# Performance work log

Measured on AMD Instinct MI355X. Metric: run time of the kernel, lower is better.

The kernel has to match this reference:

```python
import jax, jax.numpy as jnp
import numpy as np

EPS = 1e-5
GROUPS = 32
NH = 4


def group_norm(x, gamma, beta, groups=GROUPS, eps=EPS):
    # x: (B, C, H, W); normalize over (C//groups, H, W) per group
    B, C, H, W = x.shape
    xg = x.reshape(B, groups, C // groups, H, W)
    mean = xg.mean(axis=(2, 3, 4), keepdims=True)
    var = xg.var(axis=(2, 3, 4), keepdims=True)
    xn = ((xg - mean) * jax.lax.rsqrt(var + eps)).reshape(B, C, H, W)
    return xn * gamma[None, :, None, None] + beta[None, :, None, None]


def conv1x1(x, w, b):
    # x: (B, Cin, H, W), w: (Cout, Cin), b: (Cout,)
    return jnp.einsum('bchw,oc->bohw', x, w) + b[None, :, None, None]


def setup_inputs() -> dict:
    key = jax.random.key(0)
    ks = jax.random.split(key, 16)
    B, C, H, W = 4, 256, 64, 64
    d = {}
    d['x'] = jax.random.normal(ks[0], (B, C, H, W), jnp.float32)
    d['cond'] = jax.random.normal(ks[1], (B, C, H, W), jnp.float32)
    s = 1.0 / np.sqrt(C)
    d['gn_q_w'] = jnp.ones((C,), jnp.float32)
    d['gn_q_b'] = jnp.zeros((C,), jnp.float32)
    d['gn_kv_w'] = jnp.ones((C,), jnp.float32)
    d['gn_kv_b'] = jnp.zeros((C,), jnp.float32)
    d['wq'] = jax.random.normal(ks[2], (C, C), jnp.float32) * s
    d['bq'] = jnp.zeros((C,), jnp.float32)
    d['wk'] = jax.random.normal(ks[3], (C, C), jnp.float32) * s
    d['bk'] = jnp.zeros((C,), jnp.float32)
    d['wv'] = jax.random.normal(ks[4], (C, C), jnp.float32) * s
    d['bv'] = jnp.zeros((C,), jnp.float32)
    d['wo'] = jax.random.normal(ks[5], (C, C), jnp.float32) * s
    d['bo'] = jnp.zeros((C,), jnp.float32)
    return d


def reference(x, cond, gn_q_w, gn_q_b, gn_kv_w, gn_kv_b,
              wq, bq, wk, bk, wv, bv, wo, bo):
    B, C, H, W = x.shape
    hd = C // NH
    N = H * W
    scale = hd ** -0.5
    kv_in = group_norm(cond, gn_kv_w, gn_kv_b)
    q = conv1x1(group_norm(x, gn_q_w, gn_q_b), wq, bq)
    k = conv1x1(kv_in, wk, bk)
    v = conv1x1(kv_in, wv, bv)
    # (B, nh, head_dim, N) layout as in the original
    q = q.reshape(B, NH, hd, N)
    k = k.reshape(B, NH, hd, N)
    v = v.reshape(B, NH, hd, N)
    attn = jnp.einsum('bhdn,bhdm->bhnm', q, k) * scale
    attn = jax.nn.softmax(attn, axis=-1)
    out = jnp.einsum('bhnm,bhdm->bhdn', attn, v).reshape(B, C, H, W)
    return x + conv1x1(out, wo, bo)
```

## Files before the change

### kernel.cpp

```cpp
#include <hip/hip_runtime.h>
#include <hip/hip_bf16.h>

#define B_   4
#define C_   256
#define N_   4096
#define NH_  4
#define HD_  64
#define G_   32
#define CPG_ 8
#define EPS_ 1e-5f

typedef __bf16 bf16x8 __attribute__((ext_vector_type(8)));
typedef __bf16 bf16x4 __attribute__((ext_vector_type(4)));
typedef float  f32x4  __attribute__((ext_vector_type(4)));
typedef unsigned int u32x4 __attribute__((ext_vector_type(4)));
typedef unsigned int u32x2 __attribute__((ext_vector_type(2)));

#define EXP2F(x) __builtin_amdgcn_exp2f(x)

static __device__ __forceinline__ unsigned int packbf(float a, float b) {
    __bf16 x = (__bf16)a, y = (__bf16)b;
    unsigned short ux = __builtin_bit_cast(unsigned short, x);
    unsigned short uy = __builtin_bit_cast(unsigned short, y);
    return (unsigned int)ux | ((unsigned int)uy << 16);
}

__global__ __launch_bounds__(256) void wconv_kernel(const float* __restrict__ w0,
                                                    const float* __restrict__ w1,
                                                    const float* __restrict__ w2,
                                                    const float* __restrict__ w3,
                                                    __bf16* __restrict__ dst) {
    const float* srcs[4] = {w0, w1, w2, w3};
    const float* s = srcs[blockIdx.y];
    __bf16* d = dst + (size_t)blockIdx.y * C_ * C_;
    const int i = blockIdx.x * 256 + threadIdx.x;
    float4 v = ((const float4*)s)[i];
    bf16x4 o;
    o[0] = (__bf16)v.x; o[1] = (__bf16)v.y; o[2] = (__bf16)v.z; o[3] = (__bf16)v.w;
    ((bf16x4*)d)[i] = o;
}

__global__ __launch_bounds__(1024) void gn_stats_kernel(const float* __restrict__ in0,
                                                        const float* __restrict__ in1,
                                                        const float* __restrict__ gw0,
                                                        const float* __restrict__ gb0,
                                                        const float* __restrict__ gw1,
                                                        const float* __restrict__ gb1,
                                                        float* __restrict__ stat) {
    const int which = blockIdx.y;
    const float* in = which ? in1 : in0;
    const float* gw = which ? gw1 : gw0;
    const float* gb = which ? gb1 : gb0;
    const int b = blockIdx.x / G_;
    const int g = blockIdx.x % G_;
    const int tid = threadIdx.x;
    const size_t base = ((size_t)b * C_ + g * CPG_) * N_;
    const float4* pv = (const float4*)(in + base);
    const int NC = (CPG_ * N_) / 4;

    float s = 0.f, ss = 0.f;
    #pragma unroll
    for (int i = tid; i < NC; i += 1024) {
        float4 v = pv[i];
        s  += v.x + v.y + v.z + v.w;
        ss += v.x * v.x + v.y * v.y + v.z * v.z + v.w * v.w;
    }
    #pragma unroll
    for (int m = 32; m >= 1; m >>= 1) { s += __shfl_xor(s, m); ss += __shfl_xor(ss, m); }
    __shared__ float red[32];
    const int w = tid >> 6;
    if ((tid & 63) == 0) { red[w] = s; red[16 + w] = ss; }
    __syncthreads();
    s = 0.f; ss = 0.f;
    #pragma unroll
    for (int i = 0; i < 16; i++) { s += red[i]; ss += red[16 + i]; }
    const float mean = s * (1.f / 32768.f);
    const float var  = ss * (1.f / 32768.f) - mean * mean;
    const float rinv = rsqrtf(var + EPS_);
    if (tid < CPG_) {
        const int c = g * CPG_ + tid;
        float* sp = stat + (size_t)which * 2 * B_ * C_;
        const float sc = rinv * gw[c];
        sp[b * C_ + c] = sc;
        sp[B_ * C_ + b * C_ + c] = gb[c] - mean * sc;
    }
}

__global__ __launch_bounds__(256, 4) void gn_norm_kernel(const float* __restrict__ in0,
                                                         const float* __restrict__ in1,
                                                         const float* __restrict__ stat,
                                                         __bf16* __restrict__ out0,
                                                         __bf16* __restrict__ out1) {
    const int which = blockIdx.z;
    const float* in = which ? in1 : in0;
    __bf16* out = which ? out1 : out0;
    const int n0 = blockIdx.x * 64;
    const int b  = blockIdx.y;
    const int tid = threadIdx.x;
    const int w = tid >> 6, lane = tid & 63;
    const float* scp = stat + (size_t)which * 2 * B_ * C_ + b * C_;
    const float* shp = scp + B_ * C_;

    __shared__ __bf16 Lt[64][264];

    #pragma unroll 16
    for (int p = 0; p < 64; p++) {
        const int c = p * 4 + w;
        const float v = in[((size_t)(b * C_ + c)) * N_ + n0 + lane];
        const float o = v * scp[c] + shp[c];
        const int ch = (((c >> 3) ^ (lane >> 3)) << 3) + (c & 7);
        Lt[lane][ch] = (__bf16)o;
    }
    __syncthreads();
    #pragma unroll
    for (int q = 0; q < 8; q++) {
        const int r = q * 8 + (tid >> 5);
        const int l = tid & 31;
        const int ch = (l ^ (r >> 3)) << 3;
        *(bf16x8*)(out + ((size_t)b * N_ + n0 + r) * C_ + l * 8) =
            *(const bf16x8*)(&Lt[r][ch]);
    }
}

__global__ __launch_bounds__(256, 2) void qkv_kernel(const __bf16* __restrict__ Wall,
                                                     const float* __restrict__ bq,
                                                     const float* __restrict__ bk,
                                                     const float* __restrict__ bv,
                                                     const __bf16* __restrict__ Xq,
                                                     const __bf16* __restrict__ Xkv,
                                                     __bf16* __restrict__ Qo,
                                                     __bf16* __restrict__ Ko,
                                                     __bf16* __restrict__ Vo,
                                                     float qscale) {
    const int n0 = blockIdx.x * 64;
    const int sel = blockIdx.y >> 1;
    const int m0 = (blockIdx.y & 1) * 128;
    const int b  = blockIdx.z;
    const int tid = threadIdx.x;
    const int w = tid >> 6, lane = tid & 63, quad = lane >> 4, l16 = lane & 15;
    const int wn = (w >> 1) * 32;
    const int wm = (w & 1) * 64;

    const __bf16* Wb   = Wall + (size_t)sel * C_ * C_;
    const __bf16* XT   = (sel == 0) ? Xq : Xkv;
    const float*  bias = (sel == 0) ? bq : ((sel == 1) ? bk : bv);
    const float   psc  = (sel == 0) ? qscale : 1.0f;

    __shared__ union {
        __bf16 Wl[128][264];
        __bf16 T1[64][136];
        __bf16 Tv[128][72];
    } sm;

    const __bf16* wsrc = Wb + (size_t)m0 * C_;
    #pragma unroll
    for (int i = 0; i < 16; i++) {
        const int e = i * 256 + tid;
        const int row = e >> 5;
        const int c8 = (e & 31) * 8;
        *(bf16x8*)(&sm.Wl[row][c8]) = *(const bf16x8*)(wsrc + (size_t)row * C_ + c8);
    }

    const __bf16* ap0 = XT + ((size_t)b * N_ + n0 + wn + l16) * C_ + quad * 8;
    const __bf16* ap1 = ap0 + (size_t)16 * C_;
    bf16x8 areg[2][8];
    #pragma unroll
    for (int ks = 0; ks < 8; ks++) {
        areg[0][ks] = *(const bf16x8*)(ap0 + ks * 32);
        areg[1][ks] = *(const bf16x8*)(ap1 + ks * 32);
    }

    f32x4 acc[2][4];
    #pragma unroll
    for (int qg = 0; qg < 2; qg++)
        #pragma unroll
        for (int jm = 0; jm < 4; jm++) acc[qg][jm] = (f32x4){0.f, 0.f, 0.f, 0.f};

    __syncthreads();

    #pragma unroll
    for (int ks = 0; ks < 8; ks++) {
        const int kc = ks * 32;
        #pragma unroll
        for (int jm = 0; jm < 4; jm++) {
            bf16x8 bw = *(const bf16x8*)(&sm.Wl[wm + jm * 16 + l16][kc + quad * 8]);
            acc[0][jm] = __builtin_amdgcn_mfma_f32_16x16x32_bf16(areg[0][ks], bw, acc[0][jm], 0, 0, 0);
            acc[1][jm] = __builtin_amdgcn_mfma_f32_16x16x32_bf16(areg[1][ks], bw, acc[1][jm], 0, 0, 0);
        }
    }

    if (sel == 2) {
        __syncthreads();
        #pragma unroll
        for (int qg = 0; qg < 2; qg++)
            #pragma unroll
            for (int jm = 0; jm < 4; jm++) {
                const int mm = wm + jm * 16 + l16;
                const int nn = wn + qg * 16 + quad * 4;
                const float bi = bias[m0 + mm];
                bf16x4 o;
                #pragma unroll
                for (int r = 0; r < 4; r++) o[r] = (__bf16)(acc[qg][jm][r] + bi);
                *(bf16x4*)(&sm.Tv[mm][nn]) = o;
            }
        __syncthreads();
        #pragma unroll
        for (int i = 0; i < 4; i++) {
            const int mrow = i * 32 + (tid >> 3);
            const int ch = (tid & 7) * 8;
            *(bf16x8*)(Vo + (size_t)(b * C_ + m0 + mrow) * N_ + n0 + ch) =
                *(const bf16x8*)(&sm.Tv[mrow][ch]);
        }
    } else {
        __bf16* OUTb = (sel == 0) ? Qo : Ko;
        __syncthreads();
        #pragma unroll
        for (int qg = 0; qg < 2; qg++)
            #pragma unroll
            for (int jm = 0; jm < 4; jm++) {
                const int m = m0 + wm + jm * 16 + l16;
                const float bi = bias[m];
                #pragma unroll
                for (int r = 0; r < 4; r++)
                    sm.T1[wn + qg * 16 + quad * 4 + r][wm + jm * 16 + l16] =
                        (__bf16)((acc[qg][jm][r] + bi) * psc);
            }
        __syncthreads();
        const int h0 = m0 >> 6;
        #pragma unroll
        for (int i = 0; i < 4; i++) {
            const int idx = i * 256 + tid;
            const int row = idx >> 4;
            const int c = (idx & 15) * 8;
            const int hh = h0 + (c >> 6);
            const int d = c & 63;
            *(bf16x8*)(OUTb + ((size_t)(b * NH_ + hh) * N_ + n0 + row) * HD_ + d) =
                *(const bf16x8*)(&sm.T1[row][c]);
        }
    }
}

__global__ __launch_bounds__(256, 2) void gemm_kernel(const __bf16* __restrict__ Wb,
                                                      const float* __restrict__ bias,
                                                      const __bf16* __restrict__ XT,
                                                      float* __restrict__ OUTf,
                                                      const float* __restrict__ RES) {
    const int n0 = blockIdx.x * 64;
    const int m0 = blockIdx.y * 128;
    const int b  = blockIdx.z;
    const int tid = threadIdx.x;
    const int w = tid >> 6, lane = tid & 63, quad = lane >> 4, l16 = lane & 15;
    const int wn = (w >> 1) * 32;
    const int wm = (w & 1) * 64;

    __shared__ union {
        __bf16 Wl[128][264];
        float  Tf[128][68];
    } sm;

    const __bf16* wsrc = Wb + (size_t)m0 * C_;
    #pragma unroll
    for (int i = 0; i < 16; i++) {
        const int e = i * 256 + tid;
        const int row = e >> 5;
        const int c8 = (e & 31) * 8;
        *(bf16x8*)(&sm.Wl[row][c8]) = *(const bf16x8*)(wsrc + (size_t)row * C_ + c8);
    }

    const __bf16* ap0 = XT + ((size_t)b * N_ + n0 + wn + l16) * C_ + quad * 8;
    const __bf16* ap1 = ap0 + (size_t)16 * C_;
    bf16x8 areg[2][8];
    #pragma unroll
    for (int ks = 0; ks < 8; ks++) {
        areg[0][ks] = *(const bf16x8*)(ap0 + ks * 32);
        areg[1][ks] = *(const bf16x8*)(ap1 + ks * 32);
    }

    f32x4 acc[2][4];
    #pragma unroll
    for (int qg = 0; qg < 2; qg++)
        #pragma unroll
        for (int jm = 0; jm < 4; jm++) acc[qg][jm] = (f32x4){0.f, 0.f, 0.f, 0.f};

    __syncthreads();

    #pragma unroll
    for (int ks = 0; ks < 8; ks++) {
        const int kc = ks * 32;
        #pragma unroll
        for (int jm = 0; jm < 4; jm++) {
            bf16x8 bw = *(const bf16x8*)(&sm.Wl[wm + jm * 16 + l16][kc + quad * 8]);
            acc[0][jm] = __builtin_amdgcn_mfma_f32_16x16x32_bf16(areg[0][ks], bw, acc[0][jm], 0, 0, 0);
            acc[1][jm] = __builtin_amdgcn_mfma_f32_16x16x32_bf16(areg[1][ks], bw, acc[1][jm], 0, 0, 0);
        }
    }

    __syncthreads();
    #pragma unroll
    for (int qg = 0; qg < 2; qg++)
        #pragma unroll
        for (int jm = 0; jm < 4; jm++) {
            const int mm = wm + jm * 16 + l16;
            const int nn = wn + qg * 16 + quad * 4;
            const float bi = bias[m0 + mm];
            f32x4 o;
            #pragma unroll
            for (int r = 0; r < 4; r++) o[r] = acc[qg][jm][r] + bi;
            *(f32x4*)(&sm.Tf[mm][nn]) = o;
        }
    __syncthreads();
    #pragma unroll
    for (int qp = 0; qp < 8; qp++) {
        const int mrow = qp * 16 + (tid >> 4);
        const int k4 = (tid & 15) * 4;
        const size_t off = (size_t)(b * C_ + m0 + mrow) * N_ + n0 + k4;
        const float4 res = *(const float4*)(RES + off);
        f32x4 v = *(const f32x4*)(&sm.Tf[mrow][k4]);
        v[0] += res.x; v[1] += res.y; v[2] += res.z; v[3] += res.w;
        *(f32x4*)(OUTf + off) = v;
    }
}

__global__ __launch_bounds__(256, 2) void attn_kernel(const __bf16* __restrict__ qT,
                                                      const __bf16* __restrict__ kT,
                                                      const __bf16* __restrict__ V,
                                                      __bf16* __restrict__ O) {
    const int flat = blockIdx.y * 32 + blockIdx.x;
    const int bh = flat & 15;
    const int qt = flat >> 4;
    const int q0 = qt * 128;
    const int b = bh >> 2, h = bh & 3;
    const int tid = threadIdx.x;
    const int w = tid >> 6, lane = tid & 63, quad = lane >> 4, l16 = lane & 15;

    __shared__ union SMem {
        struct { __bf16 K[2][64][72]; __bf16 Vt[2][64][72]; } kv;
        __bf16 Ot[128][72];
    } sm;

    const __bf16* qTb = qT + (size_t)bh * N_ * HD_;
    const __bf16* kTb = kT + (size_t)bh * N_ * HD_;
    const __bf16* Vb  = V + ((size_t)b * C_ + h * HD_) * N_;

    bf16x8 qa[2][2];
    #pragma unroll
    for (int qg = 0; qg < 2; qg++)
        #pragma unroll
        for (int kk = 0; kk < 2; kk++)
            qa[qg][kk] = *(const bf16x8*)(qTb + (size_t)(q0 + w * 32 + qg * 16 + l16) * HD_ + kk * 32 + quad * 8);

    f32x4 oacc[2][4];
    #pragma unroll
    for (int qg = 0; qg < 2; qg++)
        #pragma unroll
        for (int j = 0; j < 4; j++) oacc[qg][j] = (f32x4){0.f, 0.f, 0.f, 0.f};
    float lsum[2] = {0.f, 0.f};

    const int srow = tid >> 3;
    const int scol = (tid & 7) * 8;

    bf16x8 rk[2], rv[2];
    #pragma unroll
    for (int i = 0; i < 2; i++) {
        const int row = srow + i * 32;
        rk[i] = *(const bf16x8*)(kTb + (size_t)row * HD_ + scol);
        rv[i] = *(const bf16x8*)(Vb + (size_t)row * N_ + scol);
    }

    for (int it = 0; it < N_ / 64; it++) {
        const int cur = it & 1;
        const int nm0 = ((it + 1) * 64) & (N_ - 1);
        #pragma unroll
        for (int i = 0; i < 2; i++) {
            const int row = srow + i * 32;
            *(bf16x8*)(&sm.kv.K[cur][row][scol])  = rk[i];
            *(bf16x8*)(&sm.kv.Vt[cur][row][scol]) = rv[i];
        }
        #pragma unroll
        for (int i = 0; i < 2; i++) {
            const int row = srow + i * 32;
            rk[i] = *(const bf16x8*)(kTb + (size_t)(nm0 + row) * HD_ + scol);
            rv[i] = *(const bf16x8*)(Vb + (size_t)row * N_ + nm0 + scol);
        }
        asm volatile("s_waitcnt lgkmcnt(0)" ::: "memory");
        __builtin_amdgcn_s_barrier();
        bf16x8 kb[2][4], vb[2][4];
        #pragma unroll
        for (int kk = 0; kk < 2; kk++)
            #pragma unroll
            for (int j = 0; j < 4; j++) {
                kb[kk][j] = *(const bf16x8*)(&sm.kv.K[cur][j * 16 + l16][kk * 32 + quad * 8]);
                vb[kk][j] = *(const bf16x8*)(&sm.kv.Vt[cur][j * 16 + l16][kk * 32 + quad * 8]);
            }
        #pragma unroll
        for (int qg = 0; qg < 2; qg++) {
            f32x4 s[4];
            #pragma unroll
            for (int j = 0; j < 4; j++) s[j] = (f32x4){0.f, 0.f, 0.f, 0.f};
            #pragma unroll
            for (int kk = 0; kk < 2; kk++)
                #pragma unroll
                for (int j = 0; j < 4; j++)
                    s[j] = __builtin_amdgcn_mfma_f32_16x16x32_bf16(kb[kk][j], qa[qg][kk], s[j], 0, 0, 0);
            float p[4][4];
            float ls = 0.f;
            #pragma unroll
            for (int j = 0; j < 4; j++) {
                #pragma unroll
                for (int r = 0; r < 4; r++) p[j][r] = EXP2F(s[j][r]);
                ls += (p[j][0] + p[j][1]) + (p[j][2] + p[j][3]);
            }
            lsum[qg] += ls;
            unsigned int pk0[4], pk1[4];
            #pragma unroll
            for (int j = 0; j < 4; j++) {
                pk0[j] = packbf(p[j][0], p[j][1]);
                pk1[j] = packbf(p[j][2], p[j][3]);
            }
            #pragma unroll
            for (int kk = 0; kk < 2; kk++) {
                u32x2 t0 = __builtin_amdgcn_permlane32_swap(pk0[2 * kk], pk0[2 * kk + 1], false, false);
                u32x2 t1 = __builtin_amdgcn_permlane32_swap(pk1[2 * kk], pk1[2 * kk + 1], false, false);
                u32x2 a0 = __builtin_amdgcn_permlane16_swap(t0[0], t0[1], false, false);
                u32x2 a1 = __builtin_amdgcn_permlane16_swap(t1[0], t1[1], false, false);
                bf16x8 pb = __builtin_bit_cast(bf16x8, (u32x4){a0[0], a1[0], a0[1], a1[1]});
                #pragma unroll
                for (int jd = 0; jd < 4; jd++)
                    oacc[qg][jd] = __builtin_amdgcn_mfma_f32_16x16x32_bf16(vb[kk][jd], pb, oacc[qg][jd], 0, 0, 0);
            }
        }
    }
    float inv[2];
    #pragma unroll
    for (int qg = 0; qg < 2; qg++) {
        float l = lsum[qg];
        l += __shfl_xor(l, 16);
        l += __shfl_xor(l, 32);
        inv[qg] = 1.f / l;
    }
    __syncthreads();
    #pragma unroll
    for (int qg = 0; qg < 2; qg++) {
        #pragma unroll
        for (int jd = 0; jd < 4; jd++) {
            bf16x4 o;
            #pragma unroll
            for (int r = 0; r < 4; r++) o[r] = (__bf16)(oacc[qg][jd][r] * inv[qg]);
            *(bf16x4*)(&sm.Ot[w * 32 + qg * 16 + l16][jd * 16 + quad * 4]) = o;
        }
    }
    __syncthreads();
    __bf16* Ob = O + ((size_t)b * N_ + q0) * C_ + h * HD_;
    const int row0 = tid >> 3, chh = (tid & 7) * 8;
    #pragma unroll
    for (int i = 0; i < 4; i++) {
        const int row = row0 + i * 32;
        *(bf16x8*)(Ob + (size_t)row * C_ + chh) = *(const bf16x8*)(&sm.Ot[row][chh]);
    }
}

extern "C" void kernel_launch(void* const* d_in, const int* in_sizes, int n_in,
                              void* d_out, int out_size, void* d_ws, size_t ws_size,
                              hipStream_t stream) {
    const float* x     = (const float*)d_in[0];
    const float* cond  = (const float*)d_in[1];
    const float* gnqw  = (const float*)d_in[2];
    const float* gnqb  = (const float*)d_in[3];
    const float* gnkw  = (const float*)d_in[4];
    const float* gnkb  = (const float*)d_in[5];
    const float* wq    = (const float*)d_in[6];
    const float* bq    = (const float*)d_in[7];
    const float* wk    = (const float*)d_in[8];
    const float* bk    = (const float*)d_in[9];
    const float* wv    = (const float*)d_in[10];
    const float* bv    = (const float*)d_in[11];
    const float* wo    = (const float*)d_in[12];
    const float* bo    = (const float*)d_in[13];
    float* out = (float*)d_out;

    const size_t TEN = (size_t)B_ * C_ * N_;
    const size_t WSZ = (size_t)C_ * C_;
    __bf16* gnx   = (__bf16*)d_ws;
    __bf16* gnc   = gnx + TEN;
    __bf16* qT    = gnc + TEN;
    __bf16* kT    = qT  + TEN;
    __bf16* v     = kT  + TEN;
    __bf16* attno = v   + TEN;
    __bf16* wb    = attno + TEN;
    float*  stat  = (float*)(wb + 4 * WSZ);

    wconv_kernel<<<dim3(64, 4), 256, 0, stream>>>(wq, wk, wv, wo, wb);

    gn_stats_kernel<<<dim3(B_ * G_, 2), 1024, 0, stream>>>(x, cond, gnqw, gnqb, gnkw, gnkb, stat);
    gn_norm_kernel<<<dim3(N_ / 64, B_, 2), 256, 0, stream>>>(x, cond, stat, gnx, gnc);

    qkv_kernel<<<dim3(N_ / 64, 6, B_), 256, 0, stream>>>(wb, bq, bk, bv, gnx, gnc,
                                                         qT, kT, v,
                                                         0.125f * 1.44269504088896f);

    attn_kernel<<<dim3(32, 16), 256, 0, stream>>>(qT, kT, v, attno);

    gemm_kernel<<<dim3(N_ / 64, C_ / 128, B_), 256, 0, stream>>>(wb + 3 * WSZ, bo, attno, out, x);
}
```

Measured before the change: 237.1 us.

## Split attention along the key dimension into two halves and add a combine kernel

The attention kernel now launches twice as many blocks, each covering half of the key/value sequence. Each block writes unnormalized bf16 partial outputs and its row sums to workspace, and a new combine kernel adds the two halves and normalizes. The launch bound is raised to allow 4 blocks per CU, aiming for more parallelism and better latency hiding. The cost is an extra kernel launch, extra global traffic for the partial results, possible register pressure from the tighter bound, and some precision loss from storing partials in bf16.

Result: slower. 244.5 us (+3.1%).

```diff
diff --git a/kernel.cpp b/kernel.cpp
--- a/kernel.cpp
+++ b/kernel.cpp
@@ -313,7 +313,7 @@
     for (int qp = 0; qp < 8; qp++) {
         const int mrow = qp * 16 + (tid >> 4);
         const int k4 = (tid & 15) * 4;
-        const size_t off = (size_t)(b * C_ + m0 + mrow) * N_ + n0 + k4;
+        const size_t off = (size_t)(b * C_ + mrow + m0) * N_ + n0 + k4;
         const float4 res = *(const float4*)(RES + off);
         f32x4 v = *(const f32x4*)(&sm.Tf[mrow][k4]);
         v[0] += res.x; v[1] += res.y; v[2] += res.z; v[3] += res.w;
@@ -321,14 +321,17 @@
     }
 }
 
-__global__ __launch_bounds__(256, 2) void attn_kernel(const __bf16* __restrict__ qT,
+__global__ __launch_bounds__(256, 4) void attn_kernel(const __bf16* __restrict__ qT,
                                                       const __bf16* __restrict__ kT,
                                                       const __bf16* __restrict__ V,
-                                                      __bf16* __restrict__ O) {
+                                                      __bf16* __restrict__ Op,
+                                                      float* __restrict__ Ls) {
     const int flat = blockIdx.y * 32 + blockIdx.x;
     const int bh = flat & 15;
-    const int qt = flat >> 4;
+    const int qt = (flat >> 4) & 31;
+    const int half = flat >> 9;
     const int q0 = qt * 128;
+    const int kv0 = half * 2048;
     const int b = bh >> 2, h = bh & 3;
     const int tid = threadIdx.x;
     const int w = tid >> 6, lane = tid & 63, quad = lane >> 4, l16 = lane & 15;
@@ -363,13 +366,13 @@
     #pragma unroll
     for (int i = 0; i < 2; i++) {
         const int row = srow + i * 32;
-        rk[i] = *(const bf16x8*)(kTb + (size_t)row * HD_ + scol);
-        rv[i] = *(const bf16x8*)(Vb + (size_t)row * N_ + scol);
-    }
-
-    for (int it = 0; it < N_ / 64; it++) {
+        rk[i] = *(const bf16x8*)(kTb + (size_t)(kv0 + row) * HD_ + scol);
+        rv[i] = *(const bf16x8*)(Vb + (size_t)row * N_ + kv0 + scol);
+    }
+
+    for (int it = 0; it < 32; it++) {
         const int cur = it & 1;
-        const int nm0 = ((it + 1) * 64) & (N_ - 1);
+        const int nm0 = kv0 + (((it + 1) * 64) & 2047);
         #pragma unroll
         for (int i = 0; i < 2; i++) {
             const int row = srow + i * 32;
@@ -430,13 +433,13 @@
             }
         }
     }
-    float inv[2];
     #pragma unroll
     for (int qg = 0; qg < 2; qg++) {
         float l = lsum[qg];
         l += __shfl_xor(l, 16);
         l += __shfl_xor(l, 32);
-        inv[qg] = 1.f / l;
+        if (quad == 0)
+            Ls[(size_t)(half * 16 + bh) * N_ + q0 + w * 32 + qg * 16 + l16] = l;
     }
     __syncthreads();
     #pragma unroll
@@ -445,17 +448,43 @@
         for (int jd = 0; jd < 4; jd++) {
             bf16x4 o;
             #pragma unroll
-            for (int r = 0; r < 4; r++) o[r] = (__bf16)(oacc[qg][jd][r] * inv[qg]);
+            for (int r = 0; r < 4; r++) o[r] = (__bf16)(oacc[qg][jd][r]);
             *(bf16x4*)(&sm.Ot[w * 32 + qg * 16 + l16][jd * 16 + quad * 4]) = o;
         }
     }
     __syncthreads();
-    __bf16* Ob = O + ((size_t)b * N_ + q0) * C_ + h * HD_;
+    __bf16* Ob = Op + ((size_t)(half * 16 + bh) * N_ + q0) * HD_;
     const int row0 = tid >> 3, chh = (tid & 7) * 8;
     #pragma unroll
     for (int i = 0; i < 4; i++) {
         const int row = row0 + i * 32;
-        *(bf16x8*)(Ob + (size_t)row * C_ + chh) = *(const bf16x8*)(&sm.Ot[row][chh]);
+        *(bf16x8*)(Ob + (size_t)row * HD_ + chh) = *(const bf16x8*)(&sm.Ot[row][chh]);
+    }
+}
+
+__global__ __launch_bounds__(256) void attn_combine_kernel(const __bf16* __restrict__ Op,
+                                                           const float* __restrict__ Ls,
+                                                           __bf16* __restrict__ O) {
+    const int q0 = blockIdx.x * 64;
+    const int bh = blockIdx.y;
+    const int b = bh >> 2, h = bh & 3;
+    const int tid = threadIdx.x;
+    const __bf16* O0 = Op + ((size_t)bh * N_ + q0) * HD_;
+    const __bf16* O1 = Op + ((size_t)(16 + bh) * N_ + q0) * HD_;
+    const float* L0 = Ls + (size_t)bh * N_ + q0;
+    const float* L1 = Ls + (size_t)(16 + bh) * N_ + q0;
+    #pragma unroll
+    for (int i = 0; i < 2; i++) {
+        const int u = i * 256 + tid;
+        const int row = u >> 3, dc = (u & 7) * 8;
+        bf16x8 a = *(const bf16x8*)(O0 + (size_t)row * HD_ + dc);
+        bf16x8 c = *(const bf16x8*)(O1 + (size_t)row * HD_ + dc);
+        const float inv = 1.f / (L0[row] + L1[row]);
+        bf16x8 o;
+        #pragma unroll
+        for (int j = 0; j < 8; j++)
+            o[j] = (__bf16)(((float)a[j] + (float)c[j]) * inv);
+        *(bf16x8*)(O + ((size_t)b * N_ + q0 + row) * C_ + h * HD_ + dc) = o;
     }
 }
 
@@ -488,6 +517,8 @@
     __bf16* attno = v   + TEN;
     __bf16* wb    = attno + TEN;
     float*  stat  = (float*)(wb + 4 * WSZ);
+    float*  lsum  = stat + 2 * 2 * B_ * C_;
+    __bf16* opart = gnx;
 
     wconv_kernel<<<dim3(64, 4), 256, 0, stream>>>(wq, wk, wv, wo, wb);
 
@@ -498,7 +529,8 @@
                                                          qT, kT, v,
                                                          0.125f * 1.44269504088896f);
 
-    attn_kernel<<<dim3(32, 16), 256, 0, stream>>>(qT, kT, v, attno);
+    attn_kernel<<<dim3(32, 32), 256, 0, stream>>>(qT, kT, v, opart, lsum);
+    attn_combine_kernel<<<dim3(N_ / 64, 16), 256, 0, stream>>>(opart, lsum, attno);
 
     gemm_kernel<<<dim3(N_ / 64, C_ / 128, B_), 256, 0, stream>>>(wb + 3 * WSZ, bo, attno, out, x);
 }
```
